# Optimization experiments

Hardware: AMD Instinct MI355X
Metric: run time of the kernel (lower is better)

The kernel has to match this reference:

```python
import jax, jax.numpy as jnp
import numpy as np

N_NODES = 50000
N_EDGES = 800000
IN_F, HID_F, OUT_F = 128, 64, 32
N_GRAPHS = 128


def setup_inputs() -> dict:
    key = jax.random.key(0)
    ks = jax.random.split(key, 8)
    x = jax.random.normal(ks[0], (N_NODES, IN_F), dtype=jnp.float32)
    edge_index = jax.random.randint(ks[1], (2, N_EDGES), 0, N_NODES, dtype=jnp.int64)
    edge_features = jax.random.uniform(ks[2], (N_EDGES,), dtype=jnp.float32)
    batch = jnp.sort(jax.random.randint(ks[3], (N_NODES,), 0, N_GRAPHS, dtype=jnp.int64))
    W = jax.random.normal(ks[4], (IN_F, HID_F), dtype=jnp.float32) / np.sqrt(IN_F)
    b = jax.random.normal(ks[5], (HID_F,), dtype=jnp.float32) * 0.01
    W1 = jax.random.normal(ks[6], (HID_F, OUT_F), dtype=jnp.float32) / np.sqrt(HID_F)
    b1 = jax.random.normal(ks[7], (OUT_F,), dtype=jnp.float32) * 0.01
    return {"x": x, "edge_index": edge_index, "edge_features": edge_features,
            "batch": batch, "num_graphs": N_GRAPHS, "W": W, "b": b, "W1": W1, "b1": b1}


def _gcn_conv(x, edge_index, edge_weight, W, b):
    # Standard GCNConv: add self-loops (weight 1), symmetric normalization,
    # transform-then-aggregate.
    n = x.shape[0]
    loop = jnp.arange(n, dtype=edge_index.dtype)
    src = jnp.concatenate([edge_index[0], loop])
    dst = jnp.concatenate([edge_index[1], loop])
    ew = jnp.concatenate([edge_weight, jnp.ones((n,), edge_weight.dtype)])
    deg = jax.ops.segment_sum(ew, dst, num_segments=n)          # [N]
    dinv = jnp.where(deg > 0, jax.lax.rsqrt(deg), 0.0)
    norm = dinv[src] * ew * dinv[dst]                           # [E+N]
    h = x @ W                                                   # [N, H]
    msg = h[src] * norm[:, None]                                # gather + scale
    out = jax.ops.segment_sum(msg, dst, num_segments=n)         # scatter-add
    return out + b


def reference(x, edge_index, edge_features, batch, num_graphs, W, b, W1, b1):
    h = _gcn_conv(x, edge_index, edge_features, W, b)
    h = jnp.tanh(h)
    # dropout is identity at inference
    node_embeddings = h
    sums = jax.ops.segment_sum(h, batch, num_segments=num_graphs)           # [G, H]
    cnts = jax.ops.segment_sum(jnp.ones((h.shape[0],), h.dtype), batch,
                               num_segments=num_graphs)                      # [G]
    graph_embeddings = sums / jnp.maximum(cnts, 1.0)[:, None]
    graph_embeddings = jnp.tanh(graph_embeddings @ W1 + b1)
    return (graph_embeddings, node_embeddings)
```

## Files before the change

### kernel.cpp

```cpp
#include <hip/hip_runtime.h>
#include <hip/hip_fp16.h>
#include <math.h>

#define N_NODES  50000
#define N_EDGES  800000
#define IN_F     128
#define HID_F    64
#define OUT_F    32
#define N_GRAPHS 128
#define SCAN_BLOCKS  ((N_NODES + 255) / 256)
#define GEMM_BLOCKS  ((N_NODES + 63) / 64)
#define HISTO_BLOCKS ((N_EDGES + 255) / 256)

__global__ __launch_bounds__(256) void fused_gemm_histo(const float* __restrict__ x,
                                                        const float* __restrict__ W,
                                                        __half* __restrict__ hs_h,
                                                        const int* __restrict__ dst,
                                                        int* __restrict__ cnt,
                                                        int* __restrict__ epos) {
    __shared__ float Ws[IN_F][HID_F];
    if (blockIdx.x >= GEMM_BLOCKS) {
        int e = (blockIdx.x - GEMM_BLOCKS) * 256 + threadIdx.x;
        if (e < N_EDGES) epos[e] = atomicAdd(&cnt[dst[e]], 1);
        return;
    }

    int tid = threadIdx.x;
    for (int i = tid * 4; i < IN_F * HID_F; i += 256 * 4) {
        *(float4*)&((float*)Ws)[i] = *(const float4*)&W[i];
    }
    __syncthreads();

    int row = blockIdx.x * 64 + (tid >> 2);
    int c0  = (tid & 3) * 16;
    if (row >= N_NODES) return;

    float acc[16];
#pragma unroll
    for (int j = 0; j < 16; ++j) acc[j] = 0.0f;

    const float* xr = x + (size_t)row * IN_F;
    for (int k = 0; k < IN_F; k += 4) {
        float4 xv = *(const float4*)&xr[k];
#pragma unroll
        for (int j = 0; j < 16; ++j) {
            acc[j] += xv.x * Ws[k + 0][c0 + j];
            acc[j] += xv.y * Ws[k + 1][c0 + j];
            acc[j] += xv.z * Ws[k + 2][c0 + j];
            acc[j] += xv.w * Ws[k + 3][c0 + j];
        }
    }
    __half* hr = hs_h + (size_t)row * HID_F + c0;
#pragma unroll
    for (int j = 0; j < 16; j += 2) {
        *(__half2*)&hr[j] = __floats2half2_rn(acc[j], acc[j + 1]);
    }
}

__global__ __launch_bounds__(256) void scan_partial_kernel(const int* __restrict__ cnt,
                                                           int* __restrict__ partials) {
    __shared__ int red[4];
    int i = blockIdx.x * 256 + threadIdx.x;
    int v = (i < N_NODES) ? cnt[i] : 0;
#pragma unroll
    for (int off = 32; off; off >>= 1) v += __shfl_down(v, off, 64);
    int w = threadIdx.x >> 6;
    if ((threadIdx.x & 63) == 0) red[w] = v;
    __syncthreads();
    if (threadIdx.x == 0) partials[blockIdx.x] = red[0] + red[1] + red[2] + red[3];
}

__global__ __launch_bounds__(256) void scan_top_kernel(const int* __restrict__ partials,
                                                       int* __restrict__ ppref) {
    __shared__ int buf[256];
    int t = threadIdx.x;
    buf[t] = (t < SCAN_BLOCKS) ? partials[t] : 0;
    __syncthreads();
    for (int off = 1; off < 256; off <<= 1) {
        int v = (t >= off) ? buf[t - off] : 0;
        __syncthreads();
        buf[t] += v;
        __syncthreads();
    }
    if (t < SCAN_BLOCKS) ppref[t] = (t > 0) ? buf[t - 1] : 0;
}

__global__ __launch_bounds__(256) void scan_final_kernel(const int* __restrict__ cnt,
                                                         const int* __restrict__ ppref,
                                                         int* __restrict__ offsets) {
    __shared__ int buf[256];
    int t = threadIdx.x;
    int i = blockIdx.x * 256 + t;
    int v = (i < N_NODES) ? cnt[i] : 0;
    buf[t] = v;
    __syncthreads();
    for (int off = 1; off < 256; off <<= 1) {
        int x = (t >= off) ? buf[t - off] : 0;
        __syncthreads();
        buf[t] += x;
        __syncthreads();
    }
    if (i < N_NODES) offsets[i] = ppref[blockIdx.x] + buf[t] - v;
}

__global__ __launch_bounds__(256) void bucket_kernel(const int* __restrict__ src,
                                                     const int* __restrict__ dst,
                                                     const float* __restrict__ ew,
                                                     const int* __restrict__ epos,
                                                     const int* __restrict__ offsets,
                                                     int2* __restrict__ edat) {
    int e = blockIdx.x * 256 + threadIdx.x;
    if (e < N_EDGES) {
        int d   = dst[e];
        int pos = offsets[d] + epos[e];
        edat[pos] = make_int2(src[e], __float_as_int(ew[e]));
    }
}

__global__ __launch_bounds__(256) void degw_kernel(const int* __restrict__ offsets,
                                                   const int* __restrict__ cnt,
                                                   const int2* __restrict__ edat,
                                                   float* __restrict__ dinv) {
    int n = blockIdx.x * 256 + threadIdx.x;
    if (n >= N_NODES) return;
    int beg = offsets[n], end = beg + cnt[n];
    float s = 1.0f;
    for (int j = beg; j < end; ++j) s += __int_as_float(edat[j].y);
    dinv[n] = 1.0f / sqrtf(s);
}

__global__ __launch_bounds__(256) void aggregate_kernel(const __half* __restrict__ hs_h,
                                                        const int* __restrict__ offsets,
                                                        const int* __restrict__ cnt,
                                                        const int2* __restrict__ edat,
                                                        const float* __restrict__ dinv,
                                                        const float* __restrict__ b,
                                                        float* __restrict__ nout) {
    int node = blockIdx.x * 4 + (threadIdx.x >> 6);
    if (node >= N_NODES) return;
    int f   = threadIdx.x & 63;
    int beg = offsets[node];
    int end = beg + cnt[node];

    float acc0 = 0.0f, acc1 = 0.0f;
    int j = beg;
    for (; j + 1 < end; j += 2) {
        int2 e0 = edat[j];
        int2 e1 = edat[j + 1];
        float w0 = dinv[e0.x] * __int_as_float(e0.y);
        float w1 = dinv[e1.x] * __int_as_float(e1.y);
        acc0 += __half2float(hs_h[(size_t)e0.x * HID_F + f]) * w0;
        acc1 += __half2float(hs_h[(size_t)e1.x * HID_F + f]) * w1;
    }
    if (j < end) {
        int2 e0 = edat[j];
        acc0 += __half2float(hs_h[(size_t)e0.x * HID_F + f]) *
                (dinv[e0.x] * __int_as_float(e0.y));
    }

    float dn = dinv[node];
    float self = __half2float(hs_h[(size_t)node * HID_F + f]) * dn;
    float v = dn * (acc0 + acc1 + self) + b[f];
    nout[(size_t)node * HID_F + f] = tanhf(v);
}

__global__ void bounds_kernel(const int* __restrict__ batch, int* __restrict__ bounds) {
    int g = threadIdx.x;
    if (g > N_GRAPHS) return;
    int lo = 0, hi = N_NODES;
    while (lo < hi) {
        int m = (lo + hi) >> 1;
        if (batch[m] < g) lo = m + 1; else hi = m;
    }
    bounds[g] = lo;
}

__global__ __launch_bounds__(256) void pool_kernel(const float* __restrict__ ne,
                                                   const int* __restrict__ bounds,
                                                   const float* __restrict__ W1,
                                                   const float* __restrict__ b1,
                                                   float* __restrict__ gout) {
    __shared__ float part[4][HID_F];
    __shared__ float mean_s[HID_F];
    int g  = blockIdx.x;
    int f  = threadIdx.x & 63;
    int w  = threadIdx.x >> 6;
    int lo = bounds[g], hi = bounds[g + 1];

    float s = 0.0f;
    for (int i = lo + w; i < hi; i += 4) s += ne[(size_t)i * HID_F + f];
    part[w][f] = s;
    __syncthreads();

    if (w == 0) {
        float m   = part[0][f] + part[1][f] + part[2][f] + part[3][f];
        float cnt = (float)(hi - lo);
        mean_s[f] = m / fmaxf(cnt, 1.0f);
    }
    __syncthreads();

    int o = threadIdx.x;
    if (o < OUT_F) {
        float acc = b1[o];
        for (int k = 0; k < HID_F; ++k) acc += mean_s[k] * W1[k * OUT_F + o];
        gout[(size_t)g * OUT_F + o] = tanhf(acc);
    }
}

extern "C" void kernel_launch(void* const* d_in, const int* in_sizes, int n_in,
                              void* d_out, int out_size, void* d_ws, size_t ws_size,
                              hipStream_t stream) {
    const float* x   = (const float*)d_in[0];
    const int*   ei  = (const int*)d_in[1];
    const float* ew  = (const float*)d_in[2];
    const int*   bat = (const int*)d_in[3];
    const float* W   = (const float*)d_in[5];
    const float* b   = (const float*)d_in[6];
    const float* W1  = (const float*)d_in[7];
    const float* b1  = (const float*)d_in[8];

    const int* src = ei;
    const int* dst = ei + N_EDGES;

    float* gout = (float*)d_out;
    float* nout = (float*)d_out + (size_t)N_GRAPHS * OUT_F;

    float*  ws_f     = (float*)d_ws;
    float*  dinv     = ws_f;
    __half* hs_h     = (__half*)(ws_f + 50000);
    int*    cnt      = (int*)(ws_f + 1650000);
    int*    offsets  = (int*)(ws_f + 1700000);
    int*    partials = (int*)(ws_f + 1750000);
    int*    ppref    = (int*)(ws_f + 1750256);
    int*    epos     = (int*)(ws_f + 1750512);
    int2*   edat     = (int2*)(ws_f + 2550512);
    int*    bounds   = (int*)(ws_f + 4150512);

    hipMemsetAsync(cnt, 0, (size_t)N_NODES * sizeof(int), stream);

    fused_gemm_histo<<<GEMM_BLOCKS + HISTO_BLOCKS, 256, 0, stream>>>(
        x, W, hs_h, dst, cnt, epos);

    scan_partial_kernel<<<SCAN_BLOCKS, 256, 0, stream>>>(cnt, partials);
    scan_top_kernel<<<1, 256, 0, stream>>>(partials, ppref);
    scan_final_kernel<<<SCAN_BLOCKS, 256, 0, stream>>>(cnt, ppref, offsets);

    bucket_kernel<<<HISTO_BLOCKS, 256, 0, stream>>>(src, dst, ew, epos,
                                                    offsets, edat);

    degw_kernel<<<SCAN_BLOCKS, 256, 0, stream>>>(offsets, cnt, edat, dinv);

    aggregate_kernel<<<(N_NODES + 3) / 4, 256, 0, stream>>>(hs_h, offsets, cnt, edat,
                                                            dinv, b, nout);

    bounds_kernel<<<1, 256, 0, stream>>>(bat, bounds);
    pool_kernel<<<N_GRAPHS, 256, 0, stream>>>(nout, bounds, W1, b1, gout);
}
```

Measured before the change: 238.8 us.

## Register-block two rows per GEMM thread and split aggregation edges across half-waves

The GEMM part now computes two output rows per thread, so each shared-memory load of W feeds twice as many FMAs, and the grid is halved. The aggregation kernel now has each half of a 64-lane wave handle alternate edges, loading half2 feature pairs per lane, and then combines the halves with a cross-lane shuffle. This doubles the edges in flight per node and halves per-lane gather instructions, at the cost of more registers in the GEMM and idle lanes during the final write.

```diff
diff --git a/kernel.cpp b/kernel.cpp
--- a/kernel.cpp
+++ b/kernel.cpp
@@ -9,7 +9,7 @@
 #define OUT_F    32
 #define N_GRAPHS 128
 #define SCAN_BLOCKS  ((N_NODES + 255) / 256)
-#define GEMM_BLOCKS  ((N_NODES + 63) / 64)
+#define GEMM_BLOCKS  ((N_NODES + 127) / 128)
 #define HISTO_BLOCKS ((N_EDGES + 255) / 256)
 
 __global__ __launch_bounds__(256) void fused_gemm_histo(const float* __restrict__ x,
@@ -31,29 +31,42 @@
     }
     __syncthreads();
 
-    int row = blockIdx.x * 64 + (tid >> 2);
-    int c0  = (tid & 3) * 16;
-    if (row >= N_NODES) return;
-
-    float acc[16];
-#pragma unroll
-    for (int j = 0; j < 16; ++j) acc[j] = 0.0f;
-
-    const float* xr = x + (size_t)row * IN_F;
+    int r0 = blockIdx.x * 128 + (tid >> 2);
+    int r1 = r0 + 64;
+    int c0 = (tid & 3) * 16;
+    if (r0 >= N_NODES) return;
+    bool has1 = (r1 < N_NODES);
+
+    float acc0[16], acc1[16];
+#pragma unroll
+    for (int j = 0; j < 16; ++j) { acc0[j] = 0.0f; acc1[j] = 0.0f; }
+
+    const float* xr0 = x + (size_t)r0 * IN_F;
+    const float* xr1 = x + (size_t)r1 * IN_F;
     for (int k = 0; k < IN_F; k += 4) {
-        float4 xv = *(const float4*)&xr[k];
+        float4 xa = *(const float4*)&xr0[k];
+        float4 xb = has1 ? *(const float4*)&xr1[k] : make_float4(0, 0, 0, 0);
 #pragma unroll
         for (int j = 0; j < 16; ++j) {
-            acc[j] += xv.x * Ws[k + 0][c0 + j];
-            acc[j] += xv.y * Ws[k + 1][c0 + j];
-            acc[j] += xv.z * Ws[k + 2][c0 + j];
-            acc[j] += xv.w * Ws[k + 3][c0 + j];
+            float w0 = Ws[k + 0][c0 + j];
+            float w1 = Ws[k + 1][c0 + j];
+            float w2 = Ws[k + 2][c0 + j];
+            float w3 = Ws[k + 3][c0 + j];
+            acc0[j] += xa.x * w0 + xa.y * w1 + xa.z * w2 + xa.w * w3;
+            acc1[j] += xb.x * w0 + xb.y * w1 + xb.z * w2 + xb.w * w3;
         }
     }
-    __half* hr = hs_h + (size_t)row * HID_F + c0;
+    __half* hr0 = hs_h + (size_t)r0 * HID_F + c0;
 #pragma unroll
     for (int j = 0; j < 16; j += 2) {
-        *(__half2*)&hr[j] = __floats2half2_rn(acc[j], acc[j + 1]);
+        *(__half2*)&hr0[j] = __floats2half2_rn(acc0[j], acc0[j + 1]);
+    }
+    if (has1) {
+        __half* hr1 = hs_h + (size_t)r1 * HID_F + c0;
+#pragma unroll
+        for (int j = 0; j < 16; j += 2) {
+            *(__half2*)&hr1[j] = __floats2half2_rn(acc1[j], acc1[j + 1]);
+        }
     }
 }
 
@@ -138,30 +151,44 @@
                                                         float* __restrict__ nout) {
     int node = blockIdx.x * 4 + (threadIdx.x >> 6);
     if (node >= N_NODES) return;
-    int f   = threadIdx.x & 63;
-    int beg = offsets[node];
-    int end = beg + cnt[node];
-
-    float acc0 = 0.0f, acc1 = 0.0f;
-    int j = beg;
-    for (; j + 1 < end; j += 2) {
+    int lane = threadIdx.x & 63;
+    int half = lane >> 5;
+    int fl   = lane & 31;
+    int beg  = offsets[node];
+    int end  = beg + cnt[node];
+
+    float ax0 = 0.0f, ay0 = 0.0f, ax1 = 0.0f, ay1 = 0.0f;
+    int j = beg + half;
+    for (; j + 2 < end; j += 4) {
         int2 e0 = edat[j];
-        int2 e1 = edat[j + 1];
+        int2 e1 = edat[j + 2];
         float w0 = dinv[e0.x] * __int_as_float(e0.y);
         float w1 = dinv[e1.x] * __int_as_float(e1.y);
-        acc0 += __half2float(hs_h[(size_t)e0.x * HID_F + f]) * w0;
-        acc1 += __half2float(hs_h[(size_t)e1.x * HID_F + f]) * w1;
+        float2 h0 = __half22float2(*(const __half2*)&hs_h[(size_t)e0.x * HID_F + 2 * fl]);
+        float2 h1 = __half22float2(*(const __half2*)&hs_h[(size_t)e1.x * HID_F + 2 * fl]);
+        ax0 += h0.x * w0; ay0 += h0.y * w0;
+        ax1 += h1.x * w1; ay1 += h1.y * w1;
     }
     if (j < end) {
         int2 e0 = edat[j];
-        acc0 += __half2float(hs_h[(size_t)e0.x * HID_F + f]) *
-                (dinv[e0.x] * __int_as_float(e0.y));
-    }
-
-    float dn = dinv[node];
-    float self = __half2float(hs_h[(size_t)node * HID_F + f]) * dn;
-    float v = dn * (acc0 + acc1 + self) + b[f];
-    nout[(size_t)node * HID_F + f] = tanhf(v);
+        float w0 = dinv[e0.x] * __int_as_float(e0.y);
+        float2 h0 = __half22float2(*(const __half2*)&hs_h[(size_t)e0.x * HID_F + 2 * fl]);
+        ax0 += h0.x * w0; ay0 += h0.y * w0;
+    }
+
+    float sx = ax0 + ax1;
+    float sy = ay0 + ay1;
+    sx += __shfl_xor(sx, 32, 64);
+    sy += __shfl_xor(sy, 32, 64);
+
+    if (half == 0) {
+        float dn = dinv[node];
+        float2 hself = __half22float2(*(const __half2*)&hs_h[(size_t)node * HID_F + 2 * fl]);
+        float2 bb = *(const float2*)&b[2 * fl];
+        float vx = dn * (sx + hself.x * dn) + bb.x;
+        float vy = dn * (sy + hself.y * dn) + bb.y;
+        *(float2*)&nout[(size_t)node * HID_F + 2 * fl] = make_float2(tanhf(vx), tanhf(vy));
+    }
 }
 
 __global__ void bounds_kernel(const int* __restrict__ batch, int* __restrict__ bounds) {
```

After: 232.0 us. 2.8% less time.
